# Kernel optimization log

Hardware: AMD Instinct MI355X
Metric: run time of the kernel (lower is better)

## Reference

```python
import jax, jax.numpy as jnp
import numpy as np

N_NODES = 100000


def _add_self_loops(edge_index, n):
    loops = jnp.arange(n, dtype=edge_index.dtype)
    row = jnp.concatenate([edge_index[0], loops])
    col = jnp.concatenate([edge_index[1], loops])
    return row, col


def _gcn_norm(row, col, n):
    # symmetric normalization deg^-1/2 on A + I (PyG GCNConv default)
    deg = jax.ops.segment_sum(jnp.ones_like(col, dtype=jnp.float32), col, num_segments=n)
    dinv = jnp.where(deg > 0, jax.lax.rsqrt(deg), 0.0)
    return dinv[row] * dinv[col]  # [E']


def _gcn_conv(x, W, b, row, col, norm, n):
    xw = x @ W                                   # [N, out]
    msg = norm[:, None] * xw[row]                # gather + edge scale, [E', out]
    agg = jax.ops.segment_sum(msg, col, num_segments=n)  # scatter-add, [N, out]
    return agg + b


def setup_inputs() -> dict:
    key = jax.random.key(0)
    ks = jax.random.split(key, 10)
    n, e, f, c = N_NODES, 6400000, 128, 4
    x = jax.random.normal(ks[0], (n, f), dtype=jnp.float32)
    edge_index = jax.random.randint(ks[1], (2, e), 0, n, dtype=jnp.int64)
    def glorot(k, shp):
        lim = float(np.sqrt(6.0 / (shp[0] + shp[1])))
        return jax.random.uniform(k, shp, jnp.float32, -lim, lim)
    return {
        "x": x, "edge_index": edge_index,
        "W1": glorot(ks[2], (f, 4)), "b1": jnp.zeros((4,), jnp.float32),
        "W2": glorot(ks[3], (4, 4)), "b2": jnp.zeros((4,), jnp.float32),
        "W3": glorot(ks[4], (4, 2)), "b3": jnp.zeros((2,), jnp.float32),
        "Wc": glorot(ks[5], (2, c)), "bc": jnp.zeros((c,), jnp.float32),
    }


def reference(x, edge_index, W1, b1, W2, b2, W3, b3, Wc, bc):
    n = x.shape[0]
    row, col = _add_self_loops(edge_index, n)
    norm = _gcn_norm(row, col, n)
    y1 = jax.nn.relu(_gcn_conv(x, W1, b1, row, col, norm, n))
    y2 = jax.nn.relu(_gcn_conv(y1, W2, b2, row, col, norm, n))
    y3 = jax.nn.relu(_gcn_conv(y2, W3, b3, row, col, norm, n))
    out = y3 @ Wc + bc
    return out, y3
```

## Files before the change

### kernel.cpp

```cpp
#include <hip/hip_runtime.h>
#include <stdint.h>

#define TPB 256
#define SPAN 512
#define LSH 9
#define PART_B 256
#define PART_T 1024
#define SCAN_T 1024
#define SCAN_B 4096
#define SORT_CAP 35840



__global__ __launch_bounds__(PART_T) void p_hist(
    const int* __restrict__ col, uint32_t* __restrict__ H,
    int NB, int E, int PBE) {
    __shared__ uint32_t cnt[1024];
    for (int i = threadIdx.x; i < NB; i += PART_T) cnt[i] = 0u;
    __syncthreads();
    int blk = blockIdx.x;
    int s = blk * PBE, e = min(E, s + PBE);
    for (int i = s + threadIdx.x; i < e; i += PART_T)
        atomicAdd(&cnt[col[i] >> LSH], 1u);
    __syncthreads();
    for (int i = threadIdx.x; i < NB; i += PART_T)
        H[(size_t)i * PART_B + blk] = cnt[i];
}

__global__ __launch_bounds__(SCAN_T) void k_scan1(
    const unsigned int* __restrict__ in, unsigned int* __restrict__ partial,
    unsigned int* __restrict__ bsum, int M) {
    __shared__ unsigned int sm[SCAN_T];
    int tid  = threadIdx.x;
    int base = blockIdx.x * SCAN_B + tid * 4;
    unsigned int v0 = (base + 0 < M) ? in[base + 0] : 0u;
    unsigned int v1 = (base + 1 < M) ? in[base + 1] : 0u;
    unsigned int v2 = (base + 2 < M) ? in[base + 2] : 0u;
    unsigned int v3 = (base + 3 < M) ? in[base + 3] : 0u;
    unsigned int s = v0 + v1 + v2 + v3;
    sm[tid] = s;
    __syncthreads();
    for (int off = 1; off < SCAN_T; off <<= 1) {
        unsigned int t = (tid >= off) ? sm[tid - off] : 0u;
        __syncthreads();
        sm[tid] += t;
        __syncthreads();
    }
    unsigned int excl = sm[tid] - s;
    if (base + 0 < M) partial[base + 0] = excl;
    if (base + 1 < M) partial[base + 1] = excl + v0;
    if (base + 2 < M) partial[base + 2] = excl + v0 + v1;
    if (base + 3 < M) partial[base + 3] = excl + v0 + v1 + v2;
    if (tid == SCAN_T - 1) bsum[blockIdx.x] = sm[SCAN_T - 1];
}

__global__ void k_scan2(unsigned int* __restrict__ bsum, int nb) {
    if (threadIdx.x == 0 && blockIdx.x == 0) {
        unsigned int run = 0;
        for (int i = 0; i < nb; ++i) {
            unsigned int t = bsum[i];
            bsum[i] = run;
            run += t;
        }
    }
}

__global__ __launch_bounds__(TPB) void k_scan3(
    const unsigned int* __restrict__ partial, const unsigned int* __restrict__ bsum,
    unsigned int* __restrict__ outp, int M, int E) {
    int i = blockIdx.x * TPB + threadIdx.x;
    if (i < M) outp[i] = partial[i] + bsum[i / SCAN_B];
    if (i == 0) outp[M] = (unsigned int)E;
}

__global__ __launch_bounds__(PART_T) void p_part(
    const int* __restrict__ row, const int* __restrict__ col,
    const uint32_t* __restrict__ O, uint32_t* __restrict__ bpack,
    int NB, int E, int PBE) {
    __shared__ uint32_t cur[1024];
    int blk = blockIdx.x;
    for (int i = threadIdx.x; i < NB; i += PART_T)
        cur[i] = O[(size_t)i * PART_B + blk];
    __syncthreads();
    int s = blk * PBE, e = min(E, s + PBE);
    for (int i = s + threadIdx.x; i < e; i += PART_T) {
        int c = col[i];
        uint32_t slot = atomicAdd(&cur[c >> LSH], 1u);
        bpack[slot] = ((uint32_t)row[i] << LSH) | (uint32_t)(c & (SPAN - 1));
    }
}

extern __shared__ uint32_t sort_buf[];
__global__ __launch_bounds__(PART_T) void p_sort(
    const uint32_t* __restrict__ bpack, const uint32_t* __restrict__ O,
    int* __restrict__ csr_row, unsigned int* __restrict__ indptr,
    float* __restrict__ dinv, int NB, int N, int E) {
    __shared__ uint32_t hist[SPAN];
    __shared__ uint32_t cur[SPAN];
    int b = blockIdx.x;
    int t = threadIdx.x;
    if (t < SPAN) hist[t] = 0u;
    __syncthreads();
    uint32_t s = O[(size_t)b * PART_B];
    uint32_t e = O[(size_t)(b + 1) * PART_B];
    uint32_t W = e - s;
    for (uint32_t i = s + t; i < e; i += PART_T)
        atomicAdd(&hist[bpack[i] & (SPAN - 1)], 1u);
    __syncthreads();
    if (t < SPAN) cur[t] = hist[t];
    __syncthreads();
    for (int off = 1; off < SPAN; off <<= 1) {
        uint32_t v = (t < SPAN && t >= off) ? cur[t - off] : 0u;
        __syncthreads();
        if (t < SPAN) cur[t] += v;
        __syncthreads();
    }
    if (t < SPAN) {
        uint32_t excl = cur[t] - hist[t];
        int n = b * SPAN + t;
        if (n < N) {
            indptr[n] = s + excl;
            dinv[n]   = rsqrtf((float)(hist[t] + 1u));
            if (n == N - 1) indptr[N] = (unsigned int)E;
        }
        cur[t] = excl;
    }
    __syncthreads();
    if (W <= SORT_CAP) {
        for (uint32_t i = s + t; i < e; i += PART_T) {
            uint32_t v = bpack[i];
            uint32_t slot = atomicAdd(&cur[v & (SPAN - 1)], 1u);
            sort_buf[slot] = v >> LSH;
        }
        __syncthreads();
        for (uint32_t j = t; j < W; j += PART_T)
            csr_row[s + j] = (int)sort_buf[j];
    } else {
        for (uint32_t i = s + t; i < e; i += PART_T) {
            uint32_t v = bpack[i];
            uint32_t slot = atomicAdd(&cur[v & (SPAN - 1)], 1u);
            csr_row[s + slot] = (int)(v >> LSH);
        }
    }
}


__global__ __launch_bounds__(TPB) void k_xw1d(
    const float* __restrict__ x, const float* __restrict__ W1,
    const float* __restrict__ dinv, float* __restrict__ dxw1, int N) {
    __shared__ float sW[512];
    for (int t = threadIdx.x; t < 512; t += TPB) sW[t] = W1[t];
    __syncthreads();
    int gid  = blockIdx.x * TPB + threadIdx.x;
    int node = gid >> 6;
    int lane = threadIdx.x & 63;
    if (node >= N) return;
    float2 v = *(const float2*)(x + (size_t)node * 128 + 2 * lane);
    const float* w0 = &sW[(2 * lane) * 4];
    const float* w1 = &sW[(2 * lane + 1) * 4];
    float a[4];
#pragma unroll
    for (int j = 0; j < 4; ++j) a[j] = v.x * w0[j] + v.y * w1[j];
#pragma unroll
    for (int off = 32; off > 0; off >>= 1) {
#pragma unroll
        for (int j = 0; j < 4; ++j) a[j] += __shfl_down(a[j], off);
    }
    if (lane == 0) {
        float d = dinv[node];
        *(float4*)(dxw1 + (size_t)node * 4) =
            make_float4(d * a[0], d * a[1], d * a[2], d * a[3]);
    }
}

__global__ __launch_bounds__(TPB) void k_gather44(
    const unsigned int* __restrict__ indptr, const int* __restrict__ csr_row,
    const float* __restrict__ dinv, const float* __restrict__ dxw_in,
    const float* __restrict__ b, const float* __restrict__ W,
    float* __restrict__ dxw_out, int N) {
    int gid  = blockIdx.x * TPB + threadIdx.x;
    int node = gid >> 4;
    int sub  = gid & 15;
    if (node >= N) return;
    int e0 = (int)indptr[node], e1 = (int)indptr[node + 1];
    float4 acc = make_float4(0.f, 0.f, 0.f, 0.f);
    for (int j = e0 + sub; j < e1; j += 16) {
        int r = csr_row[j];
        float4 m = *(const float4*)(dxw_in + (size_t)r * 4);
        acc.x += m.x; acc.y += m.y; acc.z += m.z; acc.w += m.w;
    }
#pragma unroll
    for (int off = 1; off < 16; off <<= 1) {
        acc.x += __shfl_xor(acc.x, off);
        acc.y += __shfl_xor(acc.y, off);
        acc.z += __shfl_xor(acc.z, off);
        acc.w += __shfl_xor(acc.w, off);
    }
    if (sub == 0) {
        float d = dinv[node];
        float4 sv = *(const float4*)(dxw_in + (size_t)node * 4);
        float h0 = fmaxf(d * (acc.x + sv.x) + b[0], 0.f);
        float h1 = fmaxf(d * (acc.y + sv.y) + b[1], 0.f);
        float h2 = fmaxf(d * (acc.z + sv.z) + b[2], 0.f);
        float h3 = fmaxf(d * (acc.w + sv.w) + b[3], 0.f);
        float o[4];
#pragma unroll
        for (int j = 0; j < 4; ++j)
            o[j] = h0 * W[0 * 4 + j] + h1 * W[1 * 4 + j] +
                   h2 * W[2 * 4 + j] + h3 * W[3 * 4 + j];
        *(float4*)(dxw_out + (size_t)node * 4) =
            make_float4(d * o[0], d * o[1], d * o[2], d * o[3]);
    }
}

__global__ __launch_bounds__(TPB) void k_gather42(
    const unsigned int* __restrict__ indptr, const int* __restrict__ csr_row,
    const float* __restrict__ dinv, const float* __restrict__ dxw_in,
    const float* __restrict__ b, const float* __restrict__ W,
    float* __restrict__ dxw_out, int N) {
    int gid  = blockIdx.x * TPB + threadIdx.x;
    int node = gid >> 4;
    int sub  = gid & 15;
    if (node >= N) return;
    int e0 = (int)indptr[node], e1 = (int)indptr[node + 1];
    float4 acc = make_float4(0.f, 0.f, 0.f, 0.f);
    for (int j = e0 + sub; j < e1; j += 16) {
        int r = csr_row[j];
        float4 m = *(const float4*)(dxw_in + (size_t)r * 4);
        acc.x += m.x; acc.y += m.y; acc.z += m.z; acc.w += m.w;
    }
#pragma unroll
    for (int off = 1; off < 16; off <<= 1) {
        acc.x += __shfl_xor(acc.x, off);
        acc.y += __shfl_xor(acc.y, off);
        acc.z += __shfl_xor(acc.z, off);
        acc.w += __shfl_xor(acc.w, off);
    }
    if (sub == 0) {
        float d = dinv[node];
        float4 sv = *(const float4*)(dxw_in + (size_t)node * 4);
        float h0 = fmaxf(d * (acc.x + sv.x) + b[0], 0.f);
        float h1 = fmaxf(d * (acc.y + sv.y) + b[1], 0.f);
        float h2 = fmaxf(d * (acc.z + sv.z) + b[2], 0.f);
        float h3 = fmaxf(d * (acc.w + sv.w) + b[3], 0.f);
        float o0 = h0 * W[0] + h1 * W[2] + h2 * W[4] + h3 * W[6];
        float o1 = h0 * W[1] + h1 * W[3] + h2 * W[5] + h3 * W[7];
        *(float2*)(dxw_out + (size_t)node * 2) = make_float2(d * o0, d * o1);
    }
}

__global__ __launch_bounds__(TPB) void k_gather2out(
    const unsigned int* __restrict__ indptr, const int* __restrict__ csr_row,
    const float* __restrict__ dinv, const float* __restrict__ dxw3,
    const float* __restrict__ b3, const float* __restrict__ Wc,
    const float* __restrict__ bc,
    float* __restrict__ out, float* __restrict__ y3out, int N) {
    int gid  = blockIdx.x * TPB + threadIdx.x;
    int node = gid >> 4;
    int sub  = gid & 15;
    if (node >= N) return;
    int e0 = (int)indptr[node], e1 = (int)indptr[node + 1];
    float ax = 0.f, ay = 0.f;
    for (int j = e0 + sub; j < e1; j += 16) {
        int r = csr_row[j];
        float2 m = *(const float2*)(dxw3 + (size_t)r * 2);
        ax += m.x; ay += m.y;
    }
#pragma unroll
    for (int off = 1; off < 16; off <<= 1) {
        ax += __shfl_xor(ax, off);
        ay += __shfl_xor(ay, off);
    }
    if (sub == 0) {
        float d = dinv[node];
        float2 sv = *(const float2*)(dxw3 + (size_t)node * 2);
        float y0 = fmaxf(d * (ax + sv.x) + b3[0], 0.f);
        float y1 = fmaxf(d * (ay + sv.y) + b3[1], 0.f);
        float o[4];
#pragma unroll
        for (int j = 0; j < 4; ++j)
            o[j] = y0 * Wc[0 * 4 + j] + y1 * Wc[1 * 4 + j] + bc[j];
        *(float4*)(out + (size_t)node * 4) = make_float4(o[0], o[1], o[2], o[3]);
        *(float2*)(y3out + (size_t)node * 2) = make_float2(y0, y1);
    }
}


__global__ __launch_bounds__(TPB) void k_zero_deg(unsigned int* __restrict__ deg, int N) {
    int i = blockIdx.x * TPB + threadIdx.x;
    if (i < N) deg[i] = 0u;
}

__global__ __launch_bounds__(TPB) void k_deg(
    const int* __restrict__ col, unsigned int* __restrict__ deg, int E) {
    int e = blockIdx.x * TPB + threadIdx.x;
    if (e >= E) return;
    atomicAdd(&deg[col[e]], 1u);
}

__global__ __launch_bounds__(TPB) void k_dinv(const unsigned int* __restrict__ deg,
                                              float* __restrict__ dinv, int N) {
    int i = blockIdx.x * TPB + threadIdx.x;
    if (i < N) dinv[i] = rsqrtf((float)(deg[i] + 1u));
}

__global__ __launch_bounds__(TPB) void k_xw1(
    const float* __restrict__ x, const float* __restrict__ W1,
    const float* __restrict__ dinv,
    float* __restrict__ xw, float* __restrict__ agg, int N) {
    __shared__ float sW[512];
    for (int t = threadIdx.x; t < 512; t += TPB) sW[t] = W1[t];
    __syncthreads();
    int gid  = blockIdx.x * TPB + threadIdx.x;
    int node = gid >> 6;
    int lane = threadIdx.x & 63;
    if (node >= N) return;
    float2 v = *(const float2*)(x + (size_t)node * 128 + 2 * lane);
    const float* w0 = &sW[(2 * lane) * 4];
    const float* w1 = &sW[(2 * lane + 1) * 4];
    float a[4];
#pragma unroll
    for (int j = 0; j < 4; ++j) a[j] = v.x * w0[j] + v.y * w1[j];
#pragma unroll
    for (int off = 32; off > 0; off >>= 1) {
#pragma unroll
        for (int j = 0; j < 4; ++j) a[j] += __shfl_down(a[j], off);
    }
    if (lane == 0) {
        float d  = dinv[node];
        float d2 = d * d;
        *(float4*)(xw  + (size_t)node * 4) = make_float4(a[0], a[1], a[2], a[3]);
        *(float4*)(agg + (size_t)node * 4) =
            make_float4(d2 * a[0], d2 * a[1], d2 * a[2], d2 * a[3]);
    }
}

__global__ __launch_bounds__(TPB) void k_prop4(
    const int* __restrict__ row, const int* __restrict__ col,
    const float* __restrict__ dinv,
    const float* __restrict__ xw, float* __restrict__ agg, int E) {
    int e = blockIdx.x * TPB + threadIdx.x;
    if (e >= E) return;
    int r = row[e];
    int c = col[e];
    float nv = dinv[r] * dinv[c];
    float4 m = *(const float4*)(xw + (size_t)r * 4);
    float* a = agg + (size_t)c * 4;
    atomicAdd(a + 0, nv * m.x);
    atomicAdd(a + 1, nv * m.y);
    atomicAdd(a + 2, nv * m.z);
    atomicAdd(a + 3, nv * m.w);
}

__global__ __launch_bounds__(TPB) void k_prop2(
    const int* __restrict__ row, const int* __restrict__ col,
    const float* __restrict__ dinv,
    const float* __restrict__ xw2, float* __restrict__ agg2, int E) {
    int e = blockIdx.x * TPB + threadIdx.x;
    if (e >= E) return;
    int r = row[e];
    int c = col[e];
    float nv = dinv[r] * dinv[c];
    float2 m = *(const float2*)(xw2 + (size_t)r * 2);
    float* a = agg2 + (size_t)c * 2;
    atomicAdd(a + 0, nv * m.x);
    atomicAdd(a + 1, nv * m.y);
}

__global__ __launch_bounds__(TPB) void k_node2(
    const float* __restrict__ b1, const float* __restrict__ W2,
    const float* __restrict__ dinv,
    float* __restrict__ xw, float* __restrict__ agg, int N) {
    int i = blockIdx.x * TPB + threadIdx.x;
    if (i >= N) return;
    float4 av = *(const float4*)(agg + (size_t)i * 4);
    float h0 = fmaxf(av.x + b1[0], 0.f);
    float h1 = fmaxf(av.y + b1[1], 0.f);
    float h2 = fmaxf(av.z + b1[2], 0.f);
    float h3 = fmaxf(av.w + b1[3], 0.f);
    float o[4];
#pragma unroll
    for (int j = 0; j < 4; ++j)
        o[j] = h0 * W2[0 * 4 + j] + h1 * W2[1 * 4 + j] +
               h2 * W2[2 * 4 + j] + h3 * W2[3 * 4 + j];
    float d  = dinv[i];
    float d2 = d * d;
    *(float4*)(xw  + (size_t)i * 4) = make_float4(o[0], o[1], o[2], o[3]);
    *(float4*)(agg + (size_t)i * 4) = make_float4(d2 * o[0], d2 * o[1], d2 * o[2], d2 * o[3]);
}

__global__ __launch_bounds__(TPB) void k_node3(
    const float* __restrict__ b2, const float* __restrict__ W3,
    const float* __restrict__ dinv,
    const float* __restrict__ agg,
    float* __restrict__ xw3, float* __restrict__ agg3, int N) {
    int i = blockIdx.x * TPB + threadIdx.x;
    if (i >= N) return;
    float4 av = *(const float4*)(agg + (size_t)i * 4);
    float h0 = fmaxf(av.x + b2[0], 0.f);
    float h1 = fmaxf(av.y + b2[1], 0.f);
    float h2 = fmaxf(av.z + b2[2], 0.f);
    float h3 = fmaxf(av.w + b2[3], 0.f);
    float o0 = h0 * W3[0] + h1 * W3[2] + h2 * W3[4] + h3 * W3[6];
    float o1 = h0 * W3[1] + h1 * W3[3] + h2 * W3[5] + h3 * W3[7];
    float d  = dinv[i];
    float d2 = d * d;
    *(float2*)(xw3  + (size_t)i * 2) = make_float2(o0, o1);
    *(float2*)(agg3 + (size_t)i * 2) = make_float2(d2 * o0, d2 * o1);
}

__global__ __launch_bounds__(TPB) void k_out(
    const float* __restrict__ b3, const float* __restrict__ Wc,
    const float* __restrict__ bc,
    const float* __restrict__ agg3,
    float* __restrict__ out, float* __restrict__ y3out, int N) {
    int i = blockIdx.x * TPB + threadIdx.x;
    if (i >= N) return;
    float2 av = *(const float2*)(agg3 + (size_t)i * 2);
    float y0 = fmaxf(av.x + b3[0], 0.f);
    float y1 = fmaxf(av.y + b3[1], 0.f);
    float o[4];
#pragma unroll
    for (int j = 0; j < 4; ++j)
        o[j] = y0 * Wc[0 * 4 + j] + y1 * Wc[1 * 4 + j] + bc[j];
    *(float4*)(out + (size_t)i * 4) = make_float4(o[0], o[1], o[2], o[3]);
    *(float2*)(y3out + (size_t)i * 2) = make_float2(y0, y1);
}

extern "C" void kernel_launch(void* const* d_in, const int* in_sizes, int n_in,
                              void* d_out, int out_size, void* d_ws, size_t ws_size,
                              hipStream_t stream) {
    const float* x  = (const float*)d_in[0];
    const int*   ei = (const int*)d_in[1];
    const float* W1 = (const float*)d_in[2];
    const float* b1 = (const float*)d_in[3];
    const float* W2 = (const float*)d_in[4];
    const float* b2 = (const float*)d_in[5];
    const float* W3 = (const float*)d_in[6];
    const float* b3 = (const float*)d_in[7];
    const float* Wc = (const float*)d_in[8];
    const float* bc = (const float*)d_in[9];

    const int N = in_sizes[0] / 128;
    const int E = in_sizes[1] / 2;

    const int* row = ei;
    const int* col = ei + (size_t)E;

    const int NB  = (N + SPAN - 1) / SPAN;
    const int M   = NB * PART_B;
    const int PBE = (E + PART_B - 1) / PART_B;

    float* out   = (float*)d_out;
    float* y3out = (float*)d_out + (size_t)N * 4;

    const int nblkN = (N + TPB - 1) / TPB;
    const int nblkE = (E + TPB - 1) / TPB;
    const int nblkW = (N * 64 + TPB - 1) / TPB;
    const int nblkG = (N * 16 + TPB - 1) / TPB;
    const int nblkM = (M + 1 + TPB - 1) / TPB;
    const int nblkS = (M + SCAN_B - 1) / SCAN_B;

    size_t off = 0;
    auto carve = [&](size_t bytes) -> void* {
        void* r = (void*)((char*)d_ws + off);
        off += (bytes + 255) & ~(size_t)255;
        return r;
    };
    float*        dinv    = (float*)carve((size_t)N * 4);
    float*        dxw1    = (float*)carve((size_t)N * 4 * 4);
    float*        dxw2    = (float*)carve((size_t)N * 4 * 4);
    float*        dxw3    = (float*)carve((size_t)N * 2 * 4);
    unsigned int* indptr  = (unsigned int*)carve(((size_t)N + 1) * 4);
    uint32_t*     bsum    = (uint32_t*)carve(260 * 4);
    uint32_t*     H       = (uint32_t*)carve(((size_t)M + 1) * 4);
    uint32_t*     bpack   = (uint32_t*)carve((size_t)E * 4);
    int*          csr_row = (int*)carve((size_t)E * 4);
    bool use_bucket = (off <= ws_size) && (NB <= 1024) && (N < (1 << 23));

    if (use_bucket) {
        size_t sort_lds = (size_t)SORT_CAP * 4;
        hipFuncSetAttribute((const void*)p_sort,
                            hipFuncAttributeMaxDynamicSharedMemorySize,
                            (int)sort_lds);
        p_hist<<<PART_B, PART_T, 0, stream>>>(col, H, NB, E, PBE);
        k_scan1<<<nblkS, SCAN_T, 0, stream>>>(H, H, bsum, M);
        k_scan2<<<1, 32, 0, stream>>>(bsum, nblkS);
        k_scan3<<<nblkM, TPB, 0, stream>>>(H, bsum, H, M, E);
        p_part<<<PART_B, PART_T, 0, stream>>>(row, col, H, bpack, NB, E, PBE);
        p_sort<<<NB, PART_T, sort_lds, stream>>>(bpack, H, csr_row, indptr,
                                                 dinv, NB, N, E);
        k_xw1d<<<nblkW, TPB, 0, stream>>>(x, W1, dinv, dxw1, N);
        k_gather44<<<nblkG, TPB, 0, stream>>>(indptr, csr_row, dinv, dxw1, b1, W2, dxw2, N);
        k_gather42<<<nblkG, TPB, 0, stream>>>(indptr, csr_row, dinv, dxw2, b2, W3, dxw3, N);
        k_gather2out<<<nblkG, TPB, 0, stream>>>(indptr, csr_row, dinv, dxw3, b3, Wc, bc,
                                                out, y3out, N);
    } else {
        size_t foff = 0;
        auto fcarve = [&](size_t bytes) -> void* {
            void* r = (void*)((char*)d_ws + foff);
            foff += (bytes + 255) & ~(size_t)255;
            return r;
        };
        unsigned int* deg   = (unsigned int*)fcarve((size_t)N * 4);
        float*        fdinv = (float*)fcarve((size_t)N * 4);
        float*        xw    = (float*)fcarve((size_t)N * 4 * 4);
        float*        agg   = (float*)fcarve((size_t)N * 4 * 4);
        float*        xw3   = (float*)fcarve((size_t)N * 2 * 4);
        float*        agg3  = (float*)fcarve((size_t)N * 2 * 4);
        k_zero_deg<<<nblkN, TPB, 0, stream>>>(deg, N);
        k_deg<<<nblkE, TPB, 0, stream>>>(col, deg, E);
        k_dinv<<<nblkN, TPB, 0, stream>>>(deg, fdinv, N);
        k_xw1<<<nblkW, TPB, 0, stream>>>(x, W1, fdinv, xw, agg, N);
        k_prop4<<<nblkE, TPB, 0, stream>>>(row, col, fdinv, xw, agg, E);
        k_node2<<<nblkN, TPB, 0, stream>>>(b1, W2, fdinv, xw, agg, N);
        k_prop4<<<nblkE, TPB, 0, stream>>>(row, col, fdinv, xw, agg, E);
        k_node3<<<nblkN, TPB, 0, stream>>>(b2, W3, fdinv, agg, xw3, agg3, N);
        k_prop2<<<nblkE, TPB, 0, stream>>>(row, col, fdinv, xw3, agg3, E);
        k_out<<<nblkN, TPB, 0, stream>>>(b3, Wc, bc, agg3, out, y3out, N);
    }
}
```

Baseline: 208.6 us.

## Fuse bucket sort, XW and three GCN gathers into one persistent kernel

Replaces the per-bucket sort kernel and the four follow-on kernels (XW1, two gather layers, output gather) with a single persistent kernel. Each block keeps its bucket's sorted source indices, degree-normalization factors and weights in LDS across all three layers, and uses a software grid barrier on a global counter between layers. This removes several kernel launches and the global CSR and indptr round trips, at the cost of running only NB (~196) blocks of 1024 threads and relying on all blocks being co-resident for the spin barrier.

```diff
diff --git a/kernel.cpp b/kernel.cpp
--- a/kernel.cpp
+++ b/kernel.cpp
@@ -6,10 +6,16 @@
 #define LSH 9
 #define PART_B 256
 #define PART_T 1024
+#define MEGA_T 1024
 #define SCAN_T 1024
 #define SCAN_B 4096
 #define SORT_CAP 35840
 
+
+__global__ __launch_bounds__(256) void k_zero32(uint32_t* __restrict__ p, int n) {
+    int i = blockIdx.x * 256 + threadIdx.x;
+    if (i < n) p[i] = 0u;
+}
 
 
 __global__ __launch_bounds__(PART_T) void p_hist(
@@ -90,21 +96,63 @@
     }
 }
 
-extern __shared__ uint32_t sort_buf[];
-__global__ __launch_bounds__(PART_T) void p_sort(
+
+__device__ __forceinline__ void gbar(uint32_t* cnt, uint32_t target) {
+    __syncthreads();
+    if (threadIdx.x == 0) {
+        __threadfence();
+        __hip_atomic_fetch_add(cnt, 1u, __ATOMIC_ACQ_REL, __HIP_MEMORY_SCOPE_AGENT);
+        while (__hip_atomic_load(cnt, __ATOMIC_ACQUIRE, __HIP_MEMORY_SCOPE_AGENT)
+               < target) {
+            __builtin_amdgcn_s_sleep(8);
+        }
+        __threadfence();
+    }
+    __syncthreads();
+}
+
+extern __shared__ uint32_t dyn_lds[];
+__global__ __launch_bounds__(MEGA_T) void k_mega(
     const uint32_t* __restrict__ bpack, const uint32_t* __restrict__ O,
-    int* __restrict__ csr_row, unsigned int* __restrict__ indptr,
-    float* __restrict__ dinv, int NB, int N, int E) {
+    const float* __restrict__ x,
+    const float* __restrict__ W1, const float* __restrict__ b1,
+    const float* __restrict__ W2, const float* __restrict__ b2,
+    const float* __restrict__ W3, const float* __restrict__ b3,
+    const float* __restrict__ Wc, const float* __restrict__ bc,
+    float* __restrict__ dxw1, float* __restrict__ dxw2, float* __restrict__ dxw3,
+    float* __restrict__ out, float* __restrict__ y3out,
+    uint32_t* __restrict__ barcnt, int NB, int N, int E) {
     __shared__ uint32_t hist[SPAN];
+    __shared__ uint32_t starts[SPAN + 1];
     __shared__ uint32_t cur[SPAN];
+    __shared__ float    dinv_l[SPAN];
+    __shared__ float    sW1[512];
+    __shared__ float    sWs[48];
+
     int b = blockIdx.x;
     int t = threadIdx.x;
-    if (t < SPAN) hist[t] = 0u;
-    __syncthreads();
     uint32_t s = O[(size_t)b * PART_B];
     uint32_t e = O[(size_t)(b + 1) * PART_B];
     uint32_t W = e - s;
-    for (uint32_t i = s + t; i < e; i += PART_T)
+    bool fits = (W <= (uint32_t)SORT_CAP);
+
+    if (t < 512) sW1[t] = W1[t];
+    if (t >= 512 && t < 560) {
+        int i = t - 512;
+        float v;
+        if (i < 16)      v = W2[i];
+        else if (i < 24) v = W3[i - 16];
+        else if (i < 32) v = Wc[i - 24];
+        else if (i < 36) v = b1[i - 32];
+        else if (i < 40) v = b2[i - 36];
+        else if (i < 44) v = b3[i - 40];
+        else             v = bc[i - 44];
+        sWs[i] = v;
+    }
+    if (t < SPAN) hist[t] = 0u;
+    __syncthreads();
+
+    for (uint32_t i = s + t; i < e; i += MEGA_T)
         atomicAdd(&hist[bpack[i] & (SPAN - 1)], 1u);
     __syncthreads();
     if (t < SPAN) cur[t] = hist[t];
@@ -117,171 +165,225 @@
     }
     if (t < SPAN) {
         uint32_t excl = cur[t] - hist[t];
-        int n = b * SPAN + t;
-        if (n < N) {
-            indptr[n] = s + excl;
-            dinv[n]   = rsqrtf((float)(hist[t] + 1u));
-            if (n == N - 1) indptr[N] = (unsigned int)E;
-        }
-        cur[t] = excl;
-    }
-    __syncthreads();
-    if (W <= SORT_CAP) {
-        for (uint32_t i = s + t; i < e; i += PART_T) {
+        starts[t] = excl;
+        cur[t]    = excl;
+        dinv_l[t] = rsqrtf((float)(hist[t] + 1u));
+        if (t == SPAN - 1) starts[SPAN] = excl + hist[t];
+    }
+    __syncthreads();
+    if (fits) {
+        for (uint32_t i = s + t; i < e; i += MEGA_T) {
             uint32_t v = bpack[i];
             uint32_t slot = atomicAdd(&cur[v & (SPAN - 1)], 1u);
-            sort_buf[slot] = v >> LSH;
-        }
-        __syncthreads();
-        for (uint32_t j = t; j < W; j += PART_T)
-            csr_row[s + j] = (int)sort_buf[j];
+            dyn_lds[slot] = v >> LSH;
+        }
+        __syncthreads();
+    }
+
+    int wid = t >> 6, lane = t & 63;
+    for (int ld = wid; ld < SPAN; ld += (MEGA_T >> 6)) {
+        int n = b * SPAN + ld;
+        if (n >= N) break;
+        float2 v = *(const float2*)(x + (size_t)n * 128 + 2 * lane);
+        const float* w0 = &sW1[(2 * lane) * 4];
+        const float* w1 = &sW1[(2 * lane + 1) * 4];
+        float a[4];
+#pragma unroll
+        for (int j = 0; j < 4; ++j) a[j] = v.x * w0[j] + v.y * w1[j];
+#pragma unroll
+        for (int off = 32; off > 0; off >>= 1) {
+#pragma unroll
+            for (int j = 0; j < 4; ++j) a[j] += __shfl_down(a[j], off);
+        }
+        if (lane == 0) {
+            float d = dinv_l[ld];
+            *(float4*)(dxw1 + (size_t)n * 4) =
+                make_float4(d * a[0], d * a[1], d * a[2], d * a[3]);
+        }
+    }
+    gbar(barcnt, (uint32_t)NB * 1u);
+
+    const int PACC = SPAN + 8;
+    if (fits) {
+        int sub = t & 15;
+        for (int ld = (t >> 4); ld < SPAN; ld += (MEGA_T >> 4)) {
+            int n = b * SPAN + ld;
+            if (n >= N) continue;
+            uint32_t e0 = starts[ld], e1 = starts[ld + 1];
+            float ax = 0.f, ay = 0.f, az = 0.f, aw = 0.f;
+            for (uint32_t j = e0 + sub; j < e1; j += 16) {
+                int r = (int)dyn_lds[j];
+                float4 m = *(const float4*)(dxw1 + (size_t)r * 4);
+                ax += m.x; ay += m.y; az += m.z; aw += m.w;
+            }
+#pragma unroll
+            for (int off = 1; off < 16; off <<= 1) {
+                ax += __shfl_xor(ax, off); ay += __shfl_xor(ay, off);
+                az += __shfl_xor(az, off); aw += __shfl_xor(aw, off);
+            }
+            if (sub == 0) {
+                float d = dinv_l[ld];
+                float4 sv = *(const float4*)(dxw1 + (size_t)n * 4);
+                float h0 = fmaxf(d * (ax + sv.x) + sWs[32], 0.f);
+                float h1 = fmaxf(d * (ay + sv.y) + sWs[33], 0.f);
+                float h2 = fmaxf(d * (az + sv.z) + sWs[34], 0.f);
+                float h3 = fmaxf(d * (aw + sv.w) + sWs[35], 0.f);
+                float o[4];
+#pragma unroll
+                for (int j = 0; j < 4; ++j)
+                    o[j] = h0 * sWs[0 + j] + h1 * sWs[4 + j] +
+                           h2 * sWs[8 + j] + h3 * sWs[12 + j];
+                *(float4*)(dxw2 + (size_t)n * 4) =
+                    make_float4(d * o[0], d * o[1], d * o[2], d * o[3]);
+            }
+        }
     } else {
-        for (uint32_t i = s + t; i < e; i += PART_T) {
+        float* facc = (float*)dyn_lds;
+        for (int i = t; i < 4 * PACC; i += MEGA_T) facc[i] = 0.f;
+        __syncthreads();
+        for (uint32_t i = s + t; i < e; i += MEGA_T) {
             uint32_t v = bpack[i];
-            uint32_t slot = atomicAdd(&cur[v & (SPAN - 1)], 1u);
-            csr_row[s + slot] = (int)(v >> LSH);
-        }
-    }
-}
-
-
-__global__ __launch_bounds__(TPB) void k_xw1d(
-    const float* __restrict__ x, const float* __restrict__ W1,
-    const float* __restrict__ dinv, float* __restrict__ dxw1, int N) {
-    __shared__ float sW[512];
-    for (int t = threadIdx.x; t < 512; t += TPB) sW[t] = W1[t];
-    __syncthreads();
-    int gid  = blockIdx.x * TPB + threadIdx.x;
-    int node = gid >> 6;
-    int lane = threadIdx.x & 63;
-    if (node >= N) return;
-    float2 v = *(const float2*)(x + (size_t)node * 128 + 2 * lane);
-    const float* w0 = &sW[(2 * lane) * 4];
-    const float* w1 = &sW[(2 * lane + 1) * 4];
-    float a[4];
-#pragma unroll
-    for (int j = 0; j < 4; ++j) a[j] = v.x * w0[j] + v.y * w1[j];
-#pragma unroll
-    for (int off = 32; off > 0; off >>= 1) {
-#pragma unroll
-        for (int j = 0; j < 4; ++j) a[j] += __shfl_down(a[j], off);
-    }
-    if (lane == 0) {
-        float d = dinv[node];
-        *(float4*)(dxw1 + (size_t)node * 4) =
-            make_float4(d * a[0], d * a[1], d * a[2], d * a[3]);
-    }
-}
-
-__global__ __launch_bounds__(TPB) void k_gather44(
-    const unsigned int* __restrict__ indptr, const int* __restrict__ csr_row,
-    const float* __restrict__ dinv, const float* __restrict__ dxw_in,
-    const float* __restrict__ b, const float* __restrict__ W,
-    float* __restrict__ dxw_out, int N) {
-    int gid  = blockIdx.x * TPB + threadIdx.x;
-    int node = gid >> 4;
-    int sub  = gid & 15;
-    if (node >= N) return;
-    int e0 = (int)indptr[node], e1 = (int)indptr[node + 1];
-    float4 acc = make_float4(0.f, 0.f, 0.f, 0.f);
-    for (int j = e0 + sub; j < e1; j += 16) {
-        int r = csr_row[j];
-        float4 m = *(const float4*)(dxw_in + (size_t)r * 4);
-        acc.x += m.x; acc.y += m.y; acc.z += m.z; acc.w += m.w;
-    }
-#pragma unroll
-    for (int off = 1; off < 16; off <<= 1) {
-        acc.x += __shfl_xor(acc.x, off);
-        acc.y += __shfl_xor(acc.y, off);
-        acc.z += __shfl_xor(acc.z, off);
-        acc.w += __shfl_xor(acc.w, off);
-    }
-    if (sub == 0) {
-        float d = dinv[node];
-        float4 sv = *(const float4*)(dxw_in + (size_t)node * 4);
-        float h0 = fmaxf(d * (acc.x + sv.x) + b[0], 0.f);
-        float h1 = fmaxf(d * (acc.y + sv.y) + b[1], 0.f);
-        float h2 = fmaxf(d * (acc.z + sv.z) + b[2], 0.f);
-        float h3 = fmaxf(d * (acc.w + sv.w) + b[3], 0.f);
-        float o[4];
-#pragma unroll
-        for (int j = 0; j < 4; ++j)
-            o[j] = h0 * W[0 * 4 + j] + h1 * W[1 * 4 + j] +
-                   h2 * W[2 * 4 + j] + h3 * W[3 * 4 + j];
-        *(float4*)(dxw_out + (size_t)node * 4) =
-            make_float4(d * o[0], d * o[1], d * o[2], d * o[3]);
-    }
-}
-
-__global__ __launch_bounds__(TPB) void k_gather42(
-    const unsigned int* __restrict__ indptr, const int* __restrict__ csr_row,
-    const float* __restrict__ dinv, const float* __restrict__ dxw_in,
-    const float* __restrict__ b, const float* __restrict__ W,
-    float* __restrict__ dxw_out, int N) {
-    int gid  = blockIdx.x * TPB + threadIdx.x;
-    int node = gid >> 4;
-    int sub  = gid & 15;
-    if (node >= N) return;
-    int e0 = (int)indptr[node], e1 = (int)indptr[node + 1];
-    float4 acc = make_float4(0.f, 0.f, 0.f, 0.f);
-    for (int j = e0 + sub; j < e1; j += 16) {
-        int r = csr_row[j];
-        float4 m = *(const float4*)(dxw_in + (size_t)r * 4);
-        acc.x += m.x; acc.y += m.y; acc.z += m.z; acc.w += m.w;
-    }
-#pragma unroll
-    for (int off = 1; off < 16; off <<= 1) {
-        acc.x += __shfl_xor(acc.x, off);
-        acc.y += __shfl_xor(acc.y, off);
-        acc.z += __shfl_xor(acc.z, off);
-        acc.w += __shfl_xor(acc.w, off);
-    }
-    if (sub == 0) {
-        float d = dinv[node];
-        float4 sv = *(const float4*)(dxw_in + (size_t)node * 4);
-        float h0 = fmaxf(d * (acc.x + sv.x) + b[0], 0.f);
-        float h1 = fmaxf(d * (acc.y + sv.y) + b[1], 0.f);
-        float h2 = fmaxf(d * (acc.z + sv.z) + b[2], 0.f);
-        float h3 = fmaxf(d * (acc.w + sv.w) + b[3], 0.f);
-        float o0 = h0 * W[0] + h1 * W[2] + h2 * W[4] + h3 * W[6];
-        float o1 = h0 * W[1] + h1 * W[3] + h2 * W[5] + h3 * W[7];
-        *(float2*)(dxw_out + (size_t)node * 2) = make_float2(d * o0, d * o1);
-    }
-}
-
-__global__ __launch_bounds__(TPB) void k_gather2out(
-    const unsigned int* __restrict__ indptr, const int* __restrict__ csr_row,
-    const float* __restrict__ dinv, const float* __restrict__ dxw3,
-    const float* __restrict__ b3, const float* __restrict__ Wc,
-    const float* __restrict__ bc,
-    float* __restrict__ out, float* __restrict__ y3out, int N) {
-    int gid  = blockIdx.x * TPB + threadIdx.x;
-    int node = gid >> 4;
-    int sub  = gid & 15;
-    if (node >= N) return;
-    int e0 = (int)indptr[node], e1 = (int)indptr[node + 1];
-    float ax = 0.f, ay = 0.f;
-    for (int j = e0 + sub; j < e1; j += 16) {
-        int r = csr_row[j];
-        float2 m = *(const float2*)(dxw3 + (size_t)r * 2);
-        ax += m.x; ay += m.y;
-    }
-#pragma unroll
-    for (int off = 1; off < 16; off <<= 1) {
-        ax += __shfl_xor(ax, off);
-        ay += __shfl_xor(ay, off);
-    }
-    if (sub == 0) {
-        float d = dinv[node];
-        float2 sv = *(const float2*)(dxw3 + (size_t)node * 2);
-        float y0 = fmaxf(d * (ax + sv.x) + b3[0], 0.f);
-        float y1 = fmaxf(d * (ay + sv.y) + b3[1], 0.f);
-        float o[4];
-#pragma unroll
-        for (int j = 0; j < 4; ++j)
-            o[j] = y0 * Wc[0 * 4 + j] + y1 * Wc[1 * 4 + j] + bc[j];
-        *(float4*)(out + (size_t)node * 4) = make_float4(o[0], o[1], o[2], o[3]);
-        *(float2*)(y3out + (size_t)node * 2) = make_float2(y0, y1);
+            int r = (int)(v >> LSH), ld = (int)(v & (SPAN - 1));
+            float4 m = *(const float4*)(dxw1 + (size_t)r * 4);
+            atomicAdd(&facc[0 * PACC + ld], m.x);
+            atomicAdd(&facc[1 * PACC + ld], m.y);
+            atomicAdd(&facc[2 * PACC + ld], m.z);
+            atomicAdd(&facc[3 * PACC + ld], m.w);
+        }
+        __syncthreads();
+        int n = b * SPAN + t;
+        if (t < SPAN && n < N) {
+            float d = dinv_l[t];
+            float4 sv = *(const float4*)(dxw1 + (size_t)n * 4);
+            float h0 = fmaxf(d * (facc[0 * PACC + t] + sv.x) + sWs[32], 0.f);
+            float h1 = fmaxf(d * (facc[1 * PACC + t] + sv.y) + sWs[33], 0.f);
+            float h2 = fmaxf(d * (facc[2 * PACC + t] + sv.z) + sWs[34], 0.f);
+            float h3 = fmaxf(d * (facc[3 * PACC + t] + sv.w) + sWs[35], 0.f);
+            float o[4];
+#pragma unroll
+            for (int j = 0; j < 4; ++j)
+                o[j] = h0 * sWs[0 + j] + h1 * sWs[4 + j] +
+                       h2 * sWs[8 + j] + h3 * sWs[12 + j];
+            *(float4*)(dxw2 + (size_t)n * 4) =
+                make_float4(d * o[0], d * o[1], d * o[2], d * o[3]);
+        }
+        __syncthreads();
+    }
+    gbar(barcnt, (uint32_t)NB * 2u);
+
+    if (fits) {
+        int sub = t & 15;
+        for (int ld = (t >> 4); ld < SPAN; ld += (MEGA_T >> 4)) {
+            int n = b * SPAN + ld;
+            if (n >= N) continue;
+            uint32_t e0 = starts[ld], e1 = starts[ld + 1];
+            float ax = 0.f, ay = 0.f, az = 0.f, aw = 0.f;
+            for (uint32_t j = e0 + sub; j < e1; j += 16) {
+                int r = (int)dyn_lds[j];
+                float4 m = *(const float4*)(dxw2 + (size_t)r * 4);
+                ax += m.x; ay += m.y; az += m.z; aw += m.w;
+            }
+#pragma unroll
+            for (int off = 1; off < 16; off <<= 1) {
+                ax += __shfl_xor(ax, off); ay += __shfl_xor(ay, off);
+                az += __shfl_xor(az, off); aw += __shfl_xor(aw, off);
+            }
+            if (sub == 0) {
+                float d = dinv_l[ld];
+                float4 sv = *(const float4*)(dxw2 + (size_t)n * 4);
+                float h0 = fmaxf(d * (ax + sv.x) + sWs[36], 0.f);
+                float h1 = fmaxf(d * (ay + sv.y) + sWs[37], 0.f);
+                float h2 = fmaxf(d * (az + sv.z) + sWs[38], 0.f);
+                float h3 = fmaxf(d * (aw + sv.w) + sWs[39], 0.f);
+                float o0 = h0 * sWs[16] + h1 * sWs[18] + h2 * sWs[20] + h3 * sWs[22];
+                float o1 = h0 * sWs[17] + h1 * sWs[19] + h2 * sWs[21] + h3 * sWs[23];
+                *(float2*)(dxw3 + (size_t)n * 2) = make_float2(d * o0, d * o1);
+            }
+        }
+    } else {
+        float* facc = (float*)dyn_lds;
+        for (int i = t; i < 4 * PACC; i += MEGA_T) facc[i] = 0.f;
+        __syncthreads();
+        for (uint32_t i = s + t; i < e; i += MEGA_T) {
+            uint32_t v = bpack[i];
+            int r = (int)(v >> LSH), ld = (int)(v & (SPAN - 1));
+            float4 m = *(const float4*)(dxw2 + (size_t)r * 4);
+            atomicAdd(&facc[0 * PACC + ld], m.x);
+            atomicAdd(&facc[1 * PACC + ld], m.y);
+            atomicAdd(&facc[2 * PACC + ld], m.z);
+            atomicAdd(&facc[3 * PACC + ld], m.w);
+        }
+        __syncthreads();
+        int n = b * SPAN + t;
+        if (t < SPAN && n < N) {
+            float d = dinv_l[t];
+            float4 sv = *(const float4*)(dxw2 + (size_t)n * 4);
+            float h0 = fmaxf(d * (facc[0 * PACC + t] + sv.x) + sWs[36], 0.f);
+            float h1 = fmaxf(d * (facc[1 * PACC + t] + sv.y) + sWs[37], 0.f);
+            float h2 = fmaxf(d * (facc[2 * PACC + t] + sv.z) + sWs[38], 0.f);
+            float h3 = fmaxf(d * (facc[3 * PACC + t] + sv.w) + sWs[39], 0.f);
+            float o0 = h0 * sWs[16] + h1 * sWs[18] + h2 * sWs[20] + h3 * sWs[22];
+            float o1 = h0 * sWs[17] + h1 * sWs[19] + h2 * sWs[21] + h3 * sWs[23];
+            *(float2*)(dxw3 + (size_t)n * 2) = make_float2(d * o0, d * o1);
+        }
+        __syncthreads();
+    }
+    gbar(barcnt, (uint32_t)NB * 3u);
+
+    if (fits) {
+        int sub = t & 15;
+        for (int ld = (t >> 4); ld < SPAN; ld += (MEGA_T >> 4)) {
+            int n = b * SPAN + ld;
+            if (n >= N) continue;
+            uint32_t e0 = starts[ld], e1 = starts[ld + 1];
+            float ax = 0.f, ay = 0.f;
+            for (uint32_t j = e0 + sub; j < e1; j += 16) {
+                int r = (int)dyn_lds[j];
+                float2 m = *(const float2*)(dxw3 + (size_t)r * 2);
+                ax += m.x; ay += m.y;
+            }
+#pragma unroll
+            for (int off = 1; off < 16; off <<= 1) {
+                ax += __shfl_xor(ax, off); ay += __shfl_xor(ay, off);
+            }
+            if (sub == 0) {
+                float d = dinv_l[ld];
+                float2 sv = *(const float2*)(dxw3 + (size_t)n * 2);
+                float y0 = fmaxf(d * (ax + sv.x) + sWs[40], 0.f);
+                float y1 = fmaxf(d * (ay + sv.y) + sWs[41], 0.f);
+                float o[4];
+#pragma unroll
+                for (int j = 0; j < 4; ++j)
+                    o[j] = y0 * sWs[24 + j] + y1 * sWs[28 + j] + sWs[44 + j];
+                *(float4*)(out + (size_t)n * 4) = make_float4(o[0], o[1], o[2], o[3]);
+                *(float2*)(y3out + (size_t)n * 2) = make_float2(y0, y1);
+            }
+        }
+    } else {
+        float* facc = (float*)dyn_lds;
+        for (int i = t; i < 2 * PACC; i += MEGA_T) facc[i] = 0.f;
+        __syncthreads();
+        for (uint32_t i = s + t; i < e; i += MEGA_T) {
+            uint32_t v = bpack[i];
+            int r = (int)(v >> LSH), ld = (int)(v & (SPAN - 1));
+            float2 m = *(const float2*)(dxw3 + (size_t)r * 2);
+            atomicAdd(&facc[0 * PACC + ld], m.x);
+            atomicAdd(&facc[1 * PACC + ld], m.y);
+        }
+        __syncthreads();
+        int n = b * SPAN + t;
+        if (t < SPAN && n < N) {
+            float d = dinv_l[t];
+            float2 sv = *(const float2*)(dxw3 + (size_t)n * 2);
+            float y0 = fmaxf(d * (facc[0 * PACC + t] + sv.x) + sWs[40], 0.f);
+            float y1 = fmaxf(d * (facc[1 * PACC + t] + sv.y) + sWs[41], 0.f);
+            float o[4];
+#pragma unroll
+            for (int j = 0; j < 4; ++j)
+                o[j] = y0 * sWs[24 + j] + y1 * sWs[28 + j] + sWs[44 + j];
+            *(float4*)(out + (size_t)n * 4) = make_float4(o[0], o[1], o[2], o[3]);
+            *(float2*)(y3out + (size_t)n * 2) = make_float2(y0, y1);
+        }
     }
 }
 
@@ -457,7 +559,6 @@
     const int nblkN = (N + TPB - 1) / TPB;
     const int nblkE = (E + TPB - 1) / TPB;
     const int nblkW = (N * 64 + TPB - 1) / TPB;
-    const int nblkG = (N * 16 + TPB - 1) / TPB;
     const int nblkM = (M + 1 + TPB - 1) / TPB;
     const int nblkS = (M + SCAN_B - 1) / SCAN_B;
 
@@ -467,34 +568,31 @@
         off += (bytes + 255) & ~(size_t)255;
         return r;
     };
-    float*        dinv    = (float*)carve((size_t)N * 4);
-    float*        dxw1    = (float*)carve((size_t)N * 4 * 4);
-    float*        dxw2    = (float*)carve((size_t)N * 4 * 4);
-    float*        dxw3    = (float*)carve((size_t)N * 2 * 4);
-    unsigned int* indptr  = (unsigned int*)carve(((size_t)N + 1) * 4);
-    uint32_t*     bsum    = (uint32_t*)carve(260 * 4);
-    uint32_t*     H       = (uint32_t*)carve(((size_t)M + 1) * 4);
-    uint32_t*     bpack   = (uint32_t*)carve((size_t)E * 4);
-    int*          csr_row = (int*)carve((size_t)E * 4);
-    bool use_bucket = (off <= ws_size) && (NB <= 1024) && (N < (1 << 23));
-
-    if (use_bucket) {
+    float*    dxw1   = (float*)carve((size_t)N * 4 * 4);
+    float*    dxw2   = (float*)carve((size_t)N * 4 * 4);
+    float*    dxw3   = (float*)carve((size_t)N * 2 * 4);
+    uint32_t* bsum   = (uint32_t*)carve(260 * 4);
+    uint32_t* barcnt = (uint32_t*)carve(256 * 4);
+    uint32_t* H      = (uint32_t*)carve(((size_t)M + 1) * 4);
+    uint32_t* bpack  = (uint32_t*)carve((size_t)E * 4);
+    bool use_mega = (off <= ws_size) && (NB <= 256) && (NB <= 1024) &&
+                    (N < (1 << 23));
+
+    if (use_mega) {
         size_t sort_lds = (size_t)SORT_CAP * 4;
-        hipFuncSetAttribute((const void*)p_sort,
+        hipFuncSetAttribute((const void*)k_mega,
                             hipFuncAttributeMaxDynamicSharedMemorySize,
                             (int)sort_lds);
+        k_zero32<<<1, 256, 0, stream>>>(barcnt, 256);
         p_hist<<<PART_B, PART_T, 0, stream>>>(col, H, NB, E, PBE);
         k_scan1<<<nblkS, SCAN_T, 0, stream>>>(H, H, bsum, M);
         k_scan2<<<1, 32, 0, stream>>>(bsum, nblkS);
         k_scan3<<<nblkM, TPB, 0, stream>>>(H, bsum, H, M, E);
         p_part<<<PART_B, PART_T, 0, stream>>>(row, col, H, bpack, NB, E, PBE);
-        p_sort<<<NB, PART_T, sort_lds, stream>>>(bpack, H, csr_row, indptr,
-                                                 dinv, NB, N, E);
-        k_xw1d<<<nblkW, TPB, 0, stream>>>(x, W1, dinv, dxw1, N);
-        k_gather44<<<nblkG, TPB, 0, stream>>>(indptr, csr_row, dinv, dxw1, b1, W2, dxw2, N);
-        k_gather42<<<nblkG, TPB, 0, stream>>>(indptr, csr_row, dinv, dxw2, b2, W3, dxw3, N);
-        k_gather2out<<<nblkG, TPB, 0, stream>>>(indptr, csr_row, dinv, dxw3, b3, Wc, bc,
-                                                out, y3out, N);
+        k_mega<<<NB, MEGA_T, sort_lds, stream>>>(bpack, H, x,
+                                                 W1, b1, W2, b2, W3, b3, Wc, bc,
+                                                 dxw1, dxw2, dxw3, out, y3out,
+                                                 barcnt, NB, N, E);
     } else {
         size_t foff = 0;
         auto fcarve = [&](size_t bytes) -> void* {
```

New measurement: 284.8 us. 1.37x slower.

## Split bucket sort into half-blocks and fuse first-layer X·W1 projection into it

Applied to the files above, without the earlier changes.

The per-bucket sort kernel now launches two blocks per 512-node bucket, each handling one 256-node half. This halves shared-memory use per block and doubles the number of blocks. The separate x@W1 kernel is removed, and its work runs at the end of the sort kernel for the half's nodes, using the degree histogram already in LDS. Each half-block still reads the whole bucket's bpack twice (histogram and scatter), so bucket reads double. In exchange the change gains occupancy and parallelism and drops one launch.

```diff
diff --git a/kernel.cpp b/kernel.cpp
--- a/kernel.cpp
+++ b/kernel.cpp
@@ -4,11 +4,12 @@
 #define TPB 256
 #define SPAN 512
 #define LSH 9
+#define HSPAN 256
 #define PART_B 256
 #define PART_T 1024
 #define SCAN_T 1024
 #define SCAN_B 4096
-#define SORT_CAP 35840
+#define HCAP 17408
 
 
 
@@ -91,19 +92,24 @@
 }
 
 extern __shared__ uint32_t sort_buf[];
-__global__ __launch_bounds__(PART_T) void p_sort(
+__global__ __launch_bounds__(PART_T) void p_sort_h(
     const uint32_t* __restrict__ bpack, const uint32_t* __restrict__ O,
+    const float* __restrict__ x, const float* __restrict__ W1,
     int* __restrict__ csr_row, unsigned int* __restrict__ indptr,
-    float* __restrict__ dinv, int NB, int N, int E) {
+    float* __restrict__ dinv, float* __restrict__ dxw1,
+    int NB, int N, int E) {
     __shared__ uint32_t hist[SPAN];
     __shared__ uint32_t cur[SPAN];
-    int b = blockIdx.x;
+    __shared__ uint32_t starts[SPAN + 1];
+    __shared__ float    sW1[512];
+    int j = blockIdx.x;
+    int b = j >> 1, half = j & 1;
     int t = threadIdx.x;
+    if (t < 512) sW1[t] = W1[t];
     if (t < SPAN) hist[t] = 0u;
     __syncthreads();
     uint32_t s = O[(size_t)b * PART_B];
     uint32_t e = O[(size_t)(b + 1) * PART_B];
-    uint32_t W = e - s;
     for (uint32_t i = s + t; i < e; i += PART_T)
         atomicAdd(&hist[bpack[i] & (SPAN - 1)], 1u);
     __syncthreads();
@@ -115,63 +121,67 @@
         if (t < SPAN) cur[t] += v;
         __syncthreads();
     }
-    if (t < SPAN) {
-        uint32_t excl = cur[t] - hist[t];
-        int n = b * SPAN + t;
+    if (t < SPAN) starts[t] = cur[t] - hist[t];
+    if (t == 0) starts[SPAN] = e - s;
+    __syncthreads();
+    uint32_t hbase = starts[half * HSPAN];
+    uint32_t Wh    = starts[(half + 1) * HSPAN] - hbase;
+    if (t < HSPAN) {
+        int ld = half * HSPAN + t;
+        int n  = b * SPAN + ld;
         if (n < N) {
-            indptr[n] = s + excl;
-            dinv[n]   = rsqrtf((float)(hist[t] + 1u));
+            indptr[n] = s + starts[ld];
+            dinv[n]   = rsqrtf((float)(hist[ld] + 1u));
             if (n == N - 1) indptr[N] = (unsigned int)E;
         }
-        cur[t] = excl;
-    }
-    __syncthreads();
-    if (W <= SORT_CAP) {
+    }
+    if (t < SPAN) cur[t] = starts[t] - hbase;
+    __syncthreads();
+    if (Wh <= (uint32_t)HCAP) {
         for (uint32_t i = s + t; i < e; i += PART_T) {
-            uint32_t v = bpack[i];
-            uint32_t slot = atomicAdd(&cur[v & (SPAN - 1)], 1u);
+            uint32_t v  = bpack[i];
+            uint32_t ld = v & (SPAN - 1);
+            if ((int)(ld >> 8) != half) continue;
+            uint32_t slot = atomicAdd(&cur[ld], 1u);
             sort_buf[slot] = v >> LSH;
         }
         __syncthreads();
-        for (uint32_t j = t; j < W; j += PART_T)
-            csr_row[s + j] = (int)sort_buf[j];
+        for (uint32_t k = t; k < Wh; k += PART_T)
+            csr_row[s + hbase + k] = (int)sort_buf[k];
     } else {
         for (uint32_t i = s + t; i < e; i += PART_T) {
-            uint32_t v = bpack[i];
-            uint32_t slot = atomicAdd(&cur[v & (SPAN - 1)], 1u);
-            csr_row[s + slot] = (int)(v >> LSH);
+            uint32_t v  = bpack[i];
+            uint32_t ld = v & (SPAN - 1);
+            if ((int)(ld >> 8) != half) continue;
+            uint32_t slot = atomicAdd(&cur[ld], 1u);
+            csr_row[s + hbase + slot] = (int)(v >> LSH);
         }
     }
-}
-
-
-__global__ __launch_bounds__(TPB) void k_xw1d(
-    const float* __restrict__ x, const float* __restrict__ W1,
-    const float* __restrict__ dinv, float* __restrict__ dxw1, int N) {
-    __shared__ float sW[512];
-    for (int t = threadIdx.x; t < 512; t += TPB) sW[t] = W1[t];
-    __syncthreads();
-    int gid  = blockIdx.x * TPB + threadIdx.x;
-    int node = gid >> 6;
-    int lane = threadIdx.x & 63;
-    if (node >= N) return;
-    float2 v = *(const float2*)(x + (size_t)node * 128 + 2 * lane);
-    const float* w0 = &sW[(2 * lane) * 4];
-    const float* w1 = &sW[(2 * lane + 1) * 4];
-    float a[4];
-#pragma unroll
-    for (int j = 0; j < 4; ++j) a[j] = v.x * w0[j] + v.y * w1[j];
-#pragma unroll
-    for (int off = 32; off > 0; off >>= 1) {
-#pragma unroll
-        for (int j = 0; j < 4; ++j) a[j] += __shfl_down(a[j], off);
-    }
-    if (lane == 0) {
-        float d = dinv[node];
-        *(float4*)(dxw1 + (size_t)node * 4) =
-            make_float4(d * a[0], d * a[1], d * a[2], d * a[3]);
-    }
-}
+    __syncthreads();
+    int wid = t >> 6, lane = t & 63;
+    for (int q = wid; q < HSPAN; q += (PART_T >> 6)) {
+        int ld = half * HSPAN + q;
+        int n  = b * SPAN + ld;
+        if (n >= N) break;
+        float2 v = *(const float2*)(x + (size_t)n * 128 + 2 * lane);
+        const float* w0 = &sW1[(2 * lane) * 4];
+        const float* w1 = &sW1[(2 * lane + 1) * 4];
+        float a[4];
+#pragma unroll
+        for (int jj = 0; jj < 4; ++jj) a[jj] = v.x * w0[jj] + v.y * w1[jj];
+#pragma unroll
+        for (int off = 32; off > 0; off >>= 1) {
+#pragma unroll
+            for (int jj = 0; jj < 4; ++jj) a[jj] += __shfl_down(a[jj], off);
+        }
+        if (lane == 0) {
+            float d = rsqrtf((float)(hist[ld] + 1u));
+            *(float4*)(dxw1 + (size_t)n * 4) =
+                make_float4(d * a[0], d * a[1], d * a[2], d * a[3]);
+        }
+    }
+}
+
 
 __global__ __launch_bounds__(TPB) void k_gather44(
     const unsigned int* __restrict__ indptr, const int* __restrict__ csr_row,
@@ -479,8 +489,8 @@
     bool use_bucket = (off <= ws_size) && (NB <= 1024) && (N < (1 << 23));
 
     if (use_bucket) {
-        size_t sort_lds = (size_t)SORT_CAP * 4;
-        hipFuncSetAttribute((const void*)p_sort,
+        size_t sort_lds = (size_t)HCAP * 4;
+        hipFuncSetAttribute((const void*)p_sort_h,
                             hipFuncAttributeMaxDynamicSharedMemorySize,
                             (int)sort_lds);
         p_hist<<<PART_B, PART_T, 0, stream>>>(col, H, NB, E, PBE);
@@ -488,9 +498,9 @@
         k_scan2<<<1, 32, 0, stream>>>(bsum, nblkS);
         k_scan3<<<nblkM, TPB, 0, stream>>>(H, bsum, H, M, E);
         p_part<<<PART_B, PART_T, 0, stream>>>(row, col, H, bpack, NB, E, PBE);
-        p_sort<<<NB, PART_T, sort_lds, stream>>>(bpack, H, csr_row, indptr,
-                                                 dinv, NB, N, E);
-        k_xw1d<<<nblkW, TPB, 0, stream>>>(x, W1, dinv, dxw1, N);
+        p_sort_h<<<2 * NB, PART_T, sort_lds, stream>>>(bpack, H, x, W1,
+                                                       csr_row, indptr, dinv,
+                                                       dxw1, NB, N, E);
         k_gather44<<<nblkG, TPB, 0, stream>>>(indptr, csr_row, dinv, dxw1, b1, W2, dxw2, N);
         k_gather42<<<nblkG, TPB, 0, stream>>>(indptr, csr_row, dinv, dxw2, b2, W3, dxw3, N);
         k_gather2out<<<nblkG, TPB, 0, stream>>>(indptr, csr_row, dinv, dxw3, b3, Wc, bc,
```

New measurement: 219.8 us. +5.3%, slower.
